# Kernel tuning notes

Measured on AMD Instinct MI355X. Metric: run time of the kernel, lower is better.

The kernel has to match this reference:

```python
import jax, jax.numpy as jnp
import numpy as np

N = 4096            # total nodes in batched graph
B = 64              # number of graphs
NPG = 64            # nodes per graph (N = B * NPG)
HID = 64            # hidden_dim
INIT_EMB = 32       # init_emb_dim
POS = 32            # inp_dim (positional/structural feat)
KG = 100000         # num_nodes in KG embedding table
LAYER = 3           # num_gcn_layers


def setup_inputs() -> dict:
    key = jax.random.key(0)
    ks = jax.random.split(key, 10)
    # block-diagonal symmetric binary adjacency (batched graph, no self loops)
    gi = jnp.repeat(jnp.arange(B), NPG)                      # graph_indices [N]
    block = gi[:, None] == gi[None, :]
    u = jax.random.uniform(ks[0], (N, N)) < 0.1
    a = jnp.logical_and(jnp.logical_or(u, u.T), block)
    a = a.at[jnp.arange(N), jnp.arange(N)].set(False)
    adj = a.astype(jnp.float32)
    head_ids = jnp.arange(B) * NPG           # node with ndata['id']==1 per graph
    tail_ids = jnp.arange(B) * NPG + 1       # node with ndata['id']==2 per graph
    return {
        "adj": adj,
        "feat_node": jax.random.normal(ks[1], (N, POS), jnp.float32),
        "idx": jax.random.randint(ks[2], (N,), 0, KG),
        "head_ids": head_ids,
        "tail_ids": tail_ids,
        "graph_indices": gi,
        "transform": jax.random.normal(ks[3], (INIT_EMB + POS, HID), jnp.float32) * 0.05,
        "embed": jax.random.normal(ks[4], (KG, INIT_EMB), jnp.float32) * 0.05,
        "w1": jax.random.normal(ks[5], (HID, HID), jnp.float32) * 0.01,
        "b1": jnp.zeros((HID,), jnp.float32),
        "w2": jax.random.normal(ks[6], (HID, HID), jnp.float32) * 0.01,
        "b2": jnp.zeros((HID,), jnp.float32),
        "gamma1": jnp.ones((HID,), jnp.float32),
        "beta1": jnp.zeros((HID,), jnp.float32),
        "gamma2": jnp.ones((HID,), jnp.float32),
        "beta2": jnp.zeros((HID,), jnp.float32),
    }


def _att_light(query, nodefea, mask, gamma, beta):
    # Attention_light: correlation-weighted masked aggregation + LayerNorm
    cor = jnp.abs(jnp.sum(query * nodefea, axis=-1, keepdims=True))   # [N,1]
    wei = cor * nodefea                                               # [N,H]
    num_nei = jnp.sum(mask, axis=-1, keepdims=True)                   # [N,1]
    up = jax.nn.leaky_relu(mask @ wei, negative_slope=0.01)           # [N,H]
    x = up / (num_nei + 1e-8)
    mu = jnp.mean(x, axis=-1, keepdims=True)
    var = jnp.var(x, axis=-1, keepdims=True)                          # biased, as torch LN
    return gamma * (x - mu) / jnp.sqrt(var + 1e-5) + beta


def _agg(entity, neighbor, w, b):
    # Aggregator: relu((entity + neighbor) @ w + b)
    return jax.nn.relu((entity + neighbor) @ w + b)


def reference(adj, feat_node, idx, head_ids, tail_ids, graph_indices,
              transform, embed, w1, b1, w2, b2, gamma1, beta1, gamma2, beta2):
    n = adj.shape[0]
    diag = jnp.arange(n)
    # node features: cat(struct feat, KG embedding) @ transform
    init_feat = jnp.concatenate([feat_node, embed[idx]], axis=1)      # [N, INIT+POS]
    feat = init_feat @ transform                                      # [N, H]
    # per-node query features of the opposite center
    headQ = feat[head_ids][graph_indices]                             # all_c1_featQ [N,H]
    tailQ = feat[tail_ids][graph_indices]                             # all_c2_featQ [N,H]
    # adjacency powers A_0=I, A_k = binarize(A_{k-1} @ adj, diag=1)
    A = jnp.eye(n, dtype=adj.dtype)
    flat_h = [jnp.zeros((n,), adj.dtype).at[head_ids].add(1.0)]       # sum of A_0 head rows
    flat_t = [jnp.zeros((n,), adj.dtype).at[tail_ids].add(1.0)]
    for _ in range(LAYER - 1):
        M = A @ adj
        M = M.at[diag, diag].set(1.0)
        A = (M > 0).astype(adj.dtype)
        flat_h.append(jnp.sum(A[head_ids], axis=0))
        flat_t.append(jnp.sum(A[tail_ids], axis=0))
    # initial masked features (hop-0 indicator = head/tail node indicator)
    init_head = (flat_h[0] > 0).astype(feat.dtype)[:, None] * feat
    init_tail = (flat_t[0] > 0).astype(feat.dtype)[:, None] * feat
    all_feat_head = feat
    all_feat_tail = feat
    layer_all, layer_head, layer_tail = [feat], [init_head], [init_tail]
    for hop in range(LAYER - 1, -1, -1):
        f1 = flat_h[hop]                                              # [N], 0/1 per node
        f2 = flat_t[hop]
        mask1 = f1[:, None] * adj                                     # [N,N]
        mask2 = f2[:, None] * adj
        up1 = _att_light(tailQ, all_feat_head, mask1, gamma1, beta1)
        up2 = _att_light(headQ, all_feat_tail, mask2, gamma2, beta2)
        agg1 = _agg(f1[:, None] * feat, up1, w1, b1)
        agg2 = _agg(f2[:, None] * feat, up2, w2, b2)
        all_feat_head = jnp.where((f1 > 0)[:, None], agg1, all_feat_head)
        all_feat_tail = jnp.where((f2 > 0)[:, None], agg2, all_feat_tail)
        layer_all.append(all_feat_head + all_feat_tail)
        layer_head.append(all_feat_head)
        layer_tail.append(all_feat_tail)
    # cat along feature dim then view -> stack on new axis 1
    return jnp.stack(layer_all, axis=1)                               # [N, LAYER+1, H]
```

## Files before the change

### kernel.cpp

```cpp
#include <hip/hip_runtime.h>

#define LD 68
#define XP 72

typedef float f32x4 __attribute__((ext_vector_type(4)));
typedef short s16x8 __attribute__((ext_vector_type(8)));
typedef unsigned long long u64;

__device__ __forceinline__ unsigned short f2bf(float f) {
  union { float f; unsigned int u; } v; v.f = f;
  const unsigned int r = (v.u + 0x7fffu + ((v.u >> 16) & 1u)) >> 16;
  return (unsigned short)r;
}
__device__ __forceinline__ float bf2f(unsigned short h) {
  union { unsigned int u; float f; } v; v.u = ((unsigned int)h) << 16;
  return v.f;
}

__global__ __launch_bounds__(512) void lagat_kernel(
    const float* __restrict__ adj,
    const float* __restrict__ feat_node,
    const int* __restrict__ idx,
    const int* __restrict__ head_ids,
    const int* __restrict__ tail_ids,
    const float* __restrict__ transform,
    const float* __restrict__ embed,
    const float* __restrict__ w1, const float* __restrict__ b1,
    const float* __restrict__ w2, const float* __restrict__ b2,
    const float* __restrict__ gamma1, const float* __restrict__ beta1,
    const float* __restrict__ gamma2, const float* __restrict__ beta2,
    float* __restrict__ out)
{
  __shared__ __align__(16) unsigned short CSTs[2][64][XP];
  __shared__ __align__(16) float Sb[2][64][LD];
  __shared__ __align__(16) float featb[64][LD];
  __shared__ __align__(16) float Ib[64][LD];
  __shared__ __align__(16) float Wt[2][64][LD];
  __shared__ __align__(16) float Tt[64][LD];
  __shared__ __align__(16) float prm[2][3][64];
  __shared__ u64 adjbits[64];
  __shared__ u64 lev[2][3];
  __shared__ float degs[64];

  const int g = blockIdx.x, tid = threadIdx.x, nb = g * 64;
  const int wv = tid >> 6, lane = tid & 63;
  const int ech = wv >> 2, eslab = (wv & 3) * 16;
  const int ln15 = lane & 15, lg = lane >> 4, lg4 = lg * 4;
  const int iNode = eslab + ln15;

  {
#pragma unroll
    for (int rr = 0; rr < 8; ++rr) {
      const int row = wv * 8 + rr;
      const u64 b = __ballot(adj[(size_t)(nb + row) * 4096 + nb + lane] != 0.0f);
      if (lane == 0) adjbits[row] = b;
    }
  }
  {
    const int r = tid >> 3, c8 = (tid & 7) * 8;
    if (c8 < 32) {
      const float4* fs = (const float4*)&feat_node[(size_t)(nb + r) * 32 + c8];
      *(float4*)&Ib[r][c8]     = fs[0];
      *(float4*)&Ib[r][c8 + 4] = fs[1];
    } else {
      const float4* es = (const float4*)&embed[(size_t)idx[nb + r] * 32 + (c8 - 32)];
      *(float4*)&Ib[r][c8]     = es[0];
      *(float4*)&Ib[r][c8 + 4] = es[1];
    }
  }
  {
    const int base = tid * 16;
    const int m = base >> 12, off = base & 4095;
    const int k = off >> 6, c0 = off & 63;
    const float* src = (m ? w2 : w1) + (size_t)k * 64 + c0;
#pragma unroll
    for (int u = 0; u < 4; ++u) {
      const float4 v = *(const float4*)&src[u * 4];
      Wt[m][c0 + 4 * u][k]     = v.x;
      Wt[m][c0 + 4 * u + 1][k] = v.y;
      Wt[m][c0 + 4 * u + 2][k] = v.z;
      Wt[m][c0 + 4 * u + 3][k] = v.w;
    }
  }
  {
    const int base = tid * 8;
    const int k = base >> 6, c0 = base & 63;
    const float* src = transform + (size_t)k * 64 + c0;
#pragma unroll
    for (int u = 0; u < 2; ++u) {
      const float4 v = *(const float4*)&src[u * 4];
      Tt[c0 + 4 * u][k]     = v.x;
      Tt[c0 + 4 * u + 1][k] = v.y;
      Tt[c0 + 4 * u + 2][k] = v.z;
      Tt[c0 + 4 * u + 3][k] = v.w;
    }
  }
  if (tid < 384) {
    const int a = tid >> 6, h = tid & 63;
    const float* s6 = (a == 0) ? gamma1 : (a == 1) ? beta1 : (a == 2) ? b1
                    : (a == 3) ? gamma2 : (a == 4) ? beta2 : b2;
    prm[a / 3][a % 3][h] = s6[h];
  }
  __syncthreads();

  const int hl = head_ids[g] - nb, tl = tail_ids[g] - nb;

  if (tid < 64) {
    degs[tid] = (float)__popcll(adjbits[tid]);
  } else if (tid < 192) {
    const int c = (tid >> 6) - 1;
    const int root = c ? tl : hl;
    const u64 l0 = 1ull << root;
    const u64 l1 = l0 | adjbits[root];
    u64 cand = ((l1 >> lane) & 1ull) ? adjbits[lane] : 0ull;
#pragma unroll
    for (int m = 1; m < 64; m <<= 1) cand |= __shfl_xor(cand, m, 64);
    if (lane == 0) { lev[c][0] = l0; lev[c][1] = l1; lev[c][2] = l0 | cand; }
  }
  s16x8 wfh[8], afr[2];
  {
#pragma unroll
    for (int ct = 0; ct < 4; ++ct)
#pragma unroll
      for (int ks = 0; ks < 2; ++ks) {
        const float4 v0 = *(const float4*)&Wt[ech][ct * 16 + ln15][ks * 32 + lg * 8];
        const float4 v1 = *(const float4*)&Wt[ech][ct * 16 + ln15][ks * 32 + lg * 8 + 4];
        s16x8 h;
        h[0] = (short)f2bf(v0.x); h[1] = (short)f2bf(v0.y);
        h[2] = (short)f2bf(v0.z); h[3] = (short)f2bf(v0.w);
        h[4] = (short)f2bf(v1.x); h[5] = (short)f2bf(v1.y);
        h[6] = (short)f2bf(v1.z); h[7] = (short)f2bf(v1.w);
        wfh[ct * 2 + ks] = h;
      }
    const u64 abits = adjbits[iNode];
#pragma unroll
    for (int ks = 0; ks < 2; ++ks) {
      s16x8 a;
#pragma unroll
      for (int j = 0; j < 8; ++j)
        a[j] = (short)(((abits >> (ks * 32 + lg * 8 + j)) & 1ull) ? 0x3F80 : 0);
      afr[ks] = a;
    }
  }
  if (ech == 0) {
    s16x8 ihf[2], ilf[2];
#pragma unroll
    for (int ks = 0; ks < 2; ++ks) {
      const float4 i0 = *(const float4*)&Ib[iNode][ks * 32 + lg * 8];
      const float4 i1 = *(const float4*)&Ib[iNode][ks * 32 + lg * 8 + 4];
      const float iv[8] = {i0.x, i0.y, i0.z, i0.w, i1.x, i1.y, i1.z, i1.w};
      s16x8 hh, ll;
#pragma unroll
      for (int j = 0; j < 8; ++j) {
        const unsigned short h = f2bf(iv[j]);
        hh[j] = (short)h;
        ll[j] = (short)f2bf(iv[j] - bf2f(h));
      }
      ihf[ks] = hh; ilf[ks] = ll;
    }
    f32x4 facc[4] = {{0,0,0,0},{0,0,0,0},{0,0,0,0},{0,0,0,0}};
#pragma unroll
    for (int ct = 0; ct < 4; ++ct)
#pragma unroll
      for (int ks = 0; ks < 2; ++ks) {
        const float4 t0 = *(const float4*)&Tt[ct * 16 + ln15][ks * 32 + lg * 8];
        const float4 t1 = *(const float4*)&Tt[ct * 16 + ln15][ks * 32 + lg * 8 + 4];
        s16x8 th;
        th[0] = (short)f2bf(t0.x); th[1] = (short)f2bf(t0.y);
        th[2] = (short)f2bf(t0.z); th[3] = (short)f2bf(t0.w);
        th[4] = (short)f2bf(t1.x); th[5] = (short)f2bf(t1.y);
        th[6] = (short)f2bf(t1.z); th[7] = (short)f2bf(t1.w);
        facc[ct] = __builtin_amdgcn_mfma_f32_16x16x32_bf16(th, ihf[ks], facc[ct], 0, 0, 0);
        facc[ct] = __builtin_amdgcn_mfma_f32_16x16x32_bf16(th, ilf[ks], facc[ct], 0, 0, 0);
      }
#pragma unroll
    for (int ct = 0; ct < 4; ++ct)
      *(float4*)&featb[iNode][ct * 16 + lg4] =
          make_float4(facc[ct][0], facc[ct][1], facc[ct][2], facc[ct][3]);
  }
  __syncthreads();

  {
    const int r = tid >> 3, c8 = (tid & 7) * 8;
#pragma unroll
    for (int u = 0; u < 2; ++u) {
      const float4 v = *(const float4*)&featb[r][c8 + 4 * u];
      *(float4*)&Sb[0][r][c8 + 4 * u] = v;
      *(float4*)&Sb[1][r][c8 + 4 * u] = v;
      *(float4*)&out[(size_t)(nb + r) * 256 + c8 + 4 * u] = v;
    }
  }
  const float dnv = 1.f / (degs[iNode] + 1e-8f);
  const int qrowE = ech ? hl : tl;
  u64 levCh[3];
#pragma unroll
  for (int k = 0; k < 3; ++k) levCh[k] = lev[ech][k];
  f32x4 ft4[4], qe4[4], bias4[4];
#pragma unroll
  for (int ct = 0; ct < 4; ++ct) {
    const int ebase = ((ct >> 1) << 5) + lg * 8 + ((ct & 1) << 2);
    ft4[ct] = *(const f32x4*)&featb[iNode][ebase];
    qe4[ct] = *(const f32x4*)&featb[qrowE][ct * 16 + lg4];
    bias4[ct] = *(const f32x4*)&prm[ech][2][ct * 16 + lg4];
  }
  {
    f32x4 sf4[4];
    float v = 0.f;
#pragma unroll
    for (int ct = 0; ct < 4; ++ct) {
      sf4[ct] = *(const f32x4*)&featb[iNode][ct * 16 + lg4];
#pragma unroll
      for (int r = 0; r < 4; ++r) v = fmaf(qe4[ct][r], sf4[ct][r], v);
    }
    v += __shfl_xor(v, 16); v += __shfl_xor(v, 32);
    const float vc = fabsf(v);
#pragma unroll
    for (int ct = 0; ct < 4; ++ct) {
      const int rbase = ((ct >> 1) << 5) + ((lg & 1) << 4) +
                        ((ct & 1) << 3) + ((lg >> 1) << 2);
#pragma unroll
      for (int r = 0; r < 4; ++r)
        CSTs[ech][rbase + r][iNode] = f2bf(vc * sf4[ct][r]);
    }
  }
  __syncthreads();

  const int r8 = tid >> 3, cc8 = (tid & 7) * 8;

  for (int hop = 2; hop >= 0; --hop) {
    if (hop != 2) {
      const int L = 2 - hop;
#pragma unroll
      for (int u = 0; u < 2; ++u) {
        const float4 a = *(const float4*)&Sb[0][r8][cc8 + 4 * u];
        const float4 b = *(const float4*)&Sb[1][r8][cc8 + 4 * u];
        *(float4*)&out[(size_t)(nb + r8) * 256 + (size_t)L * 64 + cc8 + 4 * u] =
            make_float4(a.x + b.x, a.y + b.y, a.z + b.z, a.w + b.w);
      }
    }

    f32x4 accB[4] = {{0,0,0,0},{0,0,0,0},{0,0,0,0},{0,0,0,0}};
#pragma unroll
    for (int ct = 0; ct < 4; ++ct)
#pragma unroll
      for (int ks = 0; ks < 2; ++ks) {
        const s16x8 ah = *(const s16x8*)&CSTs[ech][ct * 16 + ln15][ks * 32 + lg * 8];
        accB[ct] = __builtin_amdgcn_mfma_f32_16x16x32_bf16(ah, afr[ks], accB[ct], 0, 0, 0);
      }
    const float fB = (float)((levCh[hop] >> iNode) & 1ull);
    float x[4][4];
    {
      float smm = 0.f, s2m = 0.f;
#pragma unroll
      for (int ct = 0; ct < 4; ++ct)
#pragma unroll
        for (int r = 0; r < 4; ++r) {
          float z = accB[ct][r];
          z = (z > 0.f) ? z : 0.01f * z;
          z *= dnv;
          x[ct][r] = z; smm += z; s2m = fmaf(z, z, s2m);
        }
      smm += __shfl_xor(smm, 16); smm += __shfl_xor(smm, 32);
      s2m += __shfl_xor(s2m, 16); s2m += __shfl_xor(s2m, 32);
      const float mu = smm * 0.015625f;
      const float var = fmaxf(s2m * 0.015625f - mu * mu, 0.f);
      const float rstd = rsqrtf(var + 1e-5f);
#pragma unroll
      for (int ct = 0; ct < 4; ++ct) {
        const int ebase = ((ct >> 1) << 5) + lg * 8 + ((ct & 1) << 2);
        const f32x4 ga4 = *(const f32x4*)&prm[ech][0][ebase];
        const f32x4 be4 = *(const f32x4*)&prm[ech][1][ebase];
#pragma unroll
        for (int r = 0; r < 4; ++r)
          x[ct][r] = fmaf(fB, ft4[ct][r], ga4[r] * (x[ct][r] - mu) * rstd + be4[r]);
      }
    }
    s16x8 xh2[2], xl2[2];
#pragma unroll
    for (int ks = 0; ks < 2; ++ks) {
      s16x8 hh, ll;
#pragma unroll
      for (int j = 0; j < 8; ++j) {
        const float xv = x[2 * ks + (j >> 2)][j & 3];
        const unsigned short h = f2bf(xv);
        hh[j] = (short)h;
        ll[j] = (short)f2bf(xv - bf2f(h));
      }
      xh2[ks] = hh; xl2[ks] = ll;
    }
    f32x4 accE[4];
#pragma unroll
    for (int ct = 0; ct < 4; ++ct) {
      accE[ct] = bias4[ct];
#pragma unroll
      for (int ks = 0; ks < 2; ++ks) {
        accE[ct] = __builtin_amdgcn_mfma_f32_16x16x32_bf16(wfh[ct*2+ks], xh2[ks], accE[ct], 0, 0, 0);
        accE[ct] = __builtin_amdgcn_mfma_f32_16x16x32_bf16(wfh[ct*2+ks], xl2[ks], accE[ct], 0, 0, 0);
      }
    }
    float s[4][4], v = 0.f;
#pragma unroll
    for (int ct = 0; ct < 4; ++ct)
#pragma unroll
      for (int r = 0; r < 4; ++r) {
        const float sv = fmaxf(accE[ct][r], 0.f);
        s[ct][r] = sv;
        v = fmaf(qe4[ct][r], sv, v);
      }
    v += __shfl_xor(v, 16); v += __shfl_xor(v, 32);
    const float vc = fabsf(v);
    const float fE = (float)((levCh[hop] >> iNode) & 1ull);

    __syncthreads();

    if (fE != 0.f) {
#pragma unroll
      for (int ct = 0; ct < 4; ++ct) {
        *(float4*)&Sb[ech][iNode][ct * 16 + lg4] =
            make_float4(s[ct][0], s[ct][1], s[ct][2], s[ct][3]);
        if (hop) {
          const int rbase = ((ct >> 1) << 5) + ((lg & 1) << 4) +
                            ((ct & 1) << 3) + ((lg >> 1) << 2);
#pragma unroll
          for (int r = 0; r < 4; ++r)
            CSTs[ech][rbase + r][iNode] = f2bf(vc * s[ct][r]);
        }
      }
    }
    __syncthreads();
  }

  {
#pragma unroll
    for (int u = 0; u < 2; ++u) {
      const float4 a = *(const float4*)&Sb[0][r8][cc8 + 4 * u];
      const float4 b = *(const float4*)&Sb[1][r8][cc8 + 4 * u];
      *(float4*)&out[(size_t)(nb + r8) * 256 + 192 + cc8 + 4 * u] =
          make_float4(a.x + b.x, a.y + b.y, a.z + b.z, a.w + b.w);
    }
  }
}

extern "C" void kernel_launch(void* const* d_in, const int* in_sizes, int n_in,
                              void* d_out, int out_size, void* d_ws, size_t ws_size,
                              hipStream_t stream) {
  const float* adj       = (const float*)d_in[0];
  const float* feat_node = (const float*)d_in[1];
  const int*   idx       = (const int*)d_in[2];
  const int*   head_ids  = (const int*)d_in[3];
  const int*   tail_ids  = (const int*)d_in[4];
  const float* transform = (const float*)d_in[6];
  const float* embed     = (const float*)d_in[7];
  const float* w1v    = (const float*)d_in[8];
  const float* b1v    = (const float*)d_in[9];
  const float* w2v    = (const float*)d_in[10];
  const float* b2v    = (const float*)d_in[11];
  const float* gamma1 = (const float*)d_in[12];
  const float* beta1  = (const float*)d_in[13];
  const float* gamma2 = (const float*)d_in[14];
  const float* beta2  = (const float*)d_in[15];

  lagat_kernel<<<64, 512, 0, stream>>>(adj, feat_node, idx, head_ids, tail_ids,
      transform, embed, w1v, b1v, w2v, b2v, gamma1, beta1, gamma2, beta2,
      (float*)d_out);
}
```

Baseline: 18.35 us.

## Double-buffer hop state in LDS to drop one barrier per hop

The per-hop state buffers (Sb and the bf16 correlation-weighted matrix) become ping-pong buffers, with the second buffer aliased onto the weight/transform staging region that is dead by then. Each thread keeps its current node state in registers and writes the whole updated state to the next buffer unconditionally. This removes the barrier that separated reads of the old state from writes of the new one. The cost is extra unconditional LDS writes and register pressure from the carried state, plus reliance on the aliased region no longer being in use.

Result: no change. 18.62 us (+1.5%).

```diff
diff --git a/kernel.cpp b/kernel.cpp
--- a/kernel.cpp
+++ b/kernel.cpp
@@ -31,16 +31,22 @@
     const float* __restrict__ gamma2, const float* __restrict__ beta2,
     float* __restrict__ out)
 {
-  __shared__ __align__(16) unsigned short CSTs[2][64][XP];
-  __shared__ __align__(16) float Sb[2][64][LD];
+  __shared__ __align__(16) char regionB[53248];
+  __shared__ __align__(16) float Sb_A[2][64][LD];
+  __shared__ __align__(16) unsigned short CST_A[2][64][XP];
   __shared__ __align__(16) float featb[64][LD];
   __shared__ __align__(16) float Ib[64][LD];
-  __shared__ __align__(16) float Wt[2][64][LD];
-  __shared__ __align__(16) float Tt[64][LD];
   __shared__ __align__(16) float prm[2][3][64];
   __shared__ u64 adjbits[64];
   __shared__ u64 lev[2][3];
   __shared__ float degs[64];
+
+  float (*Wt)[64][LD] = reinterpret_cast<float(*)[64][LD]>(&regionB[0]);
+  float (*Tt)[LD]     = reinterpret_cast<float(*)[LD]>(&regionB[34816]);
+  float*          SbB  = reinterpret_cast<float*>(&regionB[0]);
+  unsigned short* CSTB = reinterpret_cast<unsigned short*>(&regionB[34816]);
+  float*          SbP[2]  = { &Sb_A[0][0][0], SbB };
+  unsigned short* CSTP[2] = { &CST_A[0][0][0], CSTB };
 
   const int g = blockIdx.x, tid = threadIdx.x, nb = g * 64;
   const int wv = tid >> 6, lane = tid & 63;
@@ -185,8 +191,8 @@
 #pragma unroll
     for (int u = 0; u < 2; ++u) {
       const float4 v = *(const float4*)&featb[r][c8 + 4 * u];
-      *(float4*)&Sb[0][r][c8 + 4 * u] = v;
-      *(float4*)&Sb[1][r][c8 + 4 * u] = v;
+      *(float4*)&SbP[0][(0 * 64 + r) * LD + c8 + 4 * u] = v;
+      *(float4*)&SbP[0][(1 * 64 + r) * LD + c8 + 4 * u] = v;
       *(float4*)&out[(size_t)(nb + r) * 256 + c8 + 4 * u] = v;
     }
   }
@@ -196,6 +202,8 @@
 #pragma unroll
   for (int k = 0; k < 3; ++k) levCh[k] = lev[ech][k];
   f32x4 ft4[4], qe4[4], bias4[4];
+  float s_reg[4][4];
+  float vc_reg;
 #pragma unroll
   for (int ct = 0; ct < 4; ++ct) {
     const int ebase = ((ct >> 1) << 5) + lg * 8 + ((ct & 1) << 2);
@@ -204,36 +212,42 @@
     bias4[ct] = *(const f32x4*)&prm[ech][2][ct * 16 + lg4];
   }
   {
-    f32x4 sf4[4];
     float v = 0.f;
 #pragma unroll
     for (int ct = 0; ct < 4; ++ct) {
-      sf4[ct] = *(const f32x4*)&featb[iNode][ct * 16 + lg4];
-#pragma unroll
-      for (int r = 0; r < 4; ++r) v = fmaf(qe4[ct][r], sf4[ct][r], v);
+      const f32x4 sf = *(const f32x4*)&featb[iNode][ct * 16 + lg4];
+#pragma unroll
+      for (int r = 0; r < 4; ++r) { s_reg[ct][r] = sf[r]; v = fmaf(qe4[ct][r], sf[r], v); }
     }
     v += __shfl_xor(v, 16); v += __shfl_xor(v, 32);
-    const float vc = fabsf(v);
+    vc_reg = fabsf(v);
 #pragma unroll
     for (int ct = 0; ct < 4; ++ct) {
       const int rbase = ((ct >> 1) << 5) + ((lg & 1) << 4) +
                         ((ct & 1) << 3) + ((lg >> 1) << 2);
 #pragma unroll
       for (int r = 0; r < 4; ++r)
-        CSTs[ech][rbase + r][iNode] = f2bf(vc * sf4[ct][r]);
+        CSTP[0][(ech * 64 + rbase + r) * XP + iNode] = f2bf(vc_reg * s_reg[ct][r]);
     }
   }
   __syncthreads();
 
   const int r8 = tid >> 3, cc8 = (tid & 7) * 8;
+  int cur = 0;
 
   for (int hop = 2; hop >= 0; --hop) {
+    const int nxt = cur ^ 1;
+    const float* curSb = SbP[cur];
+    const unsigned short* curCST = CSTP[cur];
+    float* nxtSb = SbP[nxt];
+    unsigned short* nxtCST = CSTP[nxt];
+
     if (hop != 2) {
       const int L = 2 - hop;
 #pragma unroll
       for (int u = 0; u < 2; ++u) {
-        const float4 a = *(const float4*)&Sb[0][r8][cc8 + 4 * u];
-        const float4 b = *(const float4*)&Sb[1][r8][cc8 + 4 * u];
+        const float4 a = *(const float4*)&curSb[(0 * 64 + r8) * LD + cc8 + 4 * u];
+        const float4 b = *(const float4*)&curSb[(1 * 64 + r8) * LD + cc8 + 4 * u];
         *(float4*)&out[(size_t)(nb + r8) * 256 + (size_t)L * 64 + cc8 + 4 * u] =
             make_float4(a.x + b.x, a.y + b.y, a.z + b.z, a.w + b.w);
       }
@@ -244,7 +258,8 @@
     for (int ct = 0; ct < 4; ++ct)
 #pragma unroll
       for (int ks = 0; ks < 2; ++ks) {
-        const s16x8 ah = *(const s16x8*)&CSTs[ech][ct * 16 + ln15][ks * 32 + lg * 8];
+        const s16x8 ah =
+            *(const s16x8*)&curCST[(ech * 64 + ct * 16 + ln15) * XP + ks * 32 + lg * 8];
         accB[ct] = __builtin_amdgcn_mfma_f32_16x16x32_bf16(ah, afr[ks], accB[ct], 0, 0, 0);
       }
     const float fB = (float)((levCh[hop] >> iNode) & 1ull);
@@ -298,43 +313,47 @@
         accE[ct] = __builtin_amdgcn_mfma_f32_16x16x32_bf16(wfh[ct*2+ks], xl2[ks], accE[ct], 0, 0, 0);
       }
     }
-    float s[4][4], v = 0.f;
+    float v = 0.f;
+    float snew[4][4];
 #pragma unroll
     for (int ct = 0; ct < 4; ++ct)
 #pragma unroll
       for (int r = 0; r < 4; ++r) {
         const float sv = fmaxf(accE[ct][r], 0.f);
-        s[ct][r] = sv;
+        snew[ct][r] = sv;
         v = fmaf(qe4[ct][r], sv, v);
       }
     v += __shfl_xor(v, 16); v += __shfl_xor(v, 32);
-    const float vc = fabsf(v);
-    const float fE = (float)((levCh[hop] >> iNode) & 1ull);
-
+    const bool upd = ((levCh[hop] >> iNode) & 1ull) != 0;
+#pragma unroll
+    for (int ct = 0; ct < 4; ++ct)
+#pragma unroll
+      for (int r = 0; r < 4; ++r)
+        s_reg[ct][r] = upd ? snew[ct][r] : s_reg[ct][r];
+    vc_reg = upd ? fabsf(v) : vc_reg;
+
+#pragma unroll
+    for (int ct = 0; ct < 4; ++ct) {
+      *(float4*)&nxtSb[(ech * 64 + iNode) * LD + ct * 16 + lg4] =
+          make_float4(s_reg[ct][0], s_reg[ct][1], s_reg[ct][2], s_reg[ct][3]);
+      if (hop) {
+        const int rbase = ((ct >> 1) << 5) + ((lg & 1) << 4) +
+                          ((ct & 1) << 3) + ((lg >> 1) << 2);
+#pragma unroll
+        for (int r = 0; r < 4; ++r)
+          nxtCST[(ech * 64 + rbase + r) * XP + iNode] = f2bf(vc_reg * s_reg[ct][r]);
+      }
+    }
     __syncthreads();
-
-    if (fE != 0.f) {
-#pragma unroll
-      for (int ct = 0; ct < 4; ++ct) {
-        *(float4*)&Sb[ech][iNode][ct * 16 + lg4] =
-            make_float4(s[ct][0], s[ct][1], s[ct][2], s[ct][3]);
-        if (hop) {
-          const int rbase = ((ct >> 1) << 5) + ((lg & 1) << 4) +
-                            ((ct & 1) << 3) + ((lg >> 1) << 2);
-#pragma unroll
-          for (int r = 0; r < 4; ++r)
-            CSTs[ech][rbase + r][iNode] = f2bf(vc * s[ct][r]);
-        }
-      }
-    }
-    __syncthreads();
-  }
-
-  {
+    cur = nxt;
+  }
+
+  {
+    const float* curSb = SbP[cur];
 #pragma unroll
     for (int u = 0; u < 2; ++u) {
-      const float4 a = *(const float4*)&Sb[0][r8][cc8 + 4 * u];
-      const float4 b = *(const float4*)&Sb[1][r8][cc8 + 4 * u];
+      const float4 a = *(const float4*)&curSb[(0 * 64 + r8) * LD + cc8 + 4 * u];
+      const float4 b = *(const float4*)&curSb[(1 * 64 + r8) * LD + cc8 + 4 * u];
       *(float4*)&out[(size_t)(nb + r8) * 256 + 192 + cc8 + 4 * u] =
           make_float4(a.x + b.x, a.y + b.y, a.z + b.z, a.w + b.w);
     }
```
